# Performance work log

Hardware: AMD Instinct MI355X
Metric: run time of the kernel (lower is better)

The kernel has to match this reference:

```python
import jax, jax.numpy as jnp
import numpy as np

N = 4096          # nodes (= Mamba sequence length)
E_EDGES = 65536   # edges
D = 512           # dim_h (= d_inner, expand=1)
NEXP = 4          # num_experts (cfg.model.num_experts)
DSTATE = 16
DCONV = 4
DTRANK = 32       # ceil(D/16)
EPS = 1e-5


def _silu(x):
    return x * jax.nn.sigmoid(x)


def _bn(h, g, b):
    # BatchNorm1d over node axis (batch statistics)
    mu = h.mean(0)
    var = h.var(0)
    return (h - mu) * jax.lax.rsqrt(var + EPS) * g + b


def _mamba(u, in_w, conv_w, conv_b, x_w, dt_w, dt_b, A_log, Dp, out_w):
    # u: [L, D] single-sequence Mamba(d_model=D, d_state=16, d_conv=4, expand=1)
    L = u.shape[0]
    xz = u @ in_w                      # [L, 2D]
    xc, z = xz[:, :D], xz[:, D:]
    xp = jnp.pad(xc, ((DCONV - 1, 0), (0, 0)))
    xconv = conv_b
    for k in range(DCONV):             # depthwise causal conv, tiny fixed loop
        xconv = xconv + conv_w[:, k] * xp[k:k + L]
    xs = _silu(xconv)                  # [L, D]
    dbc = xs @ x_w                     # [L, DTRANK + 2*DSTATE]
    dt = jax.nn.softplus(dbc[:, :DTRANK] @ dt_w + dt_b)          # [L, D]
    Bm = dbc[:, DTRANK:DTRANK + DSTATE]                          # [L, S]
    Cm = dbc[:, DTRANK + DSTATE:]                                # [L, S]
    A = -jnp.exp(A_log)                                          # [D, S]
    dA = jnp.exp(dt[:, :, None] * A[None])                       # [L, D, S]
    dBu = dt[:, :, None] * Bm[:, None, :] * xs[:, :, None]       # [L, D, S]

    def step(hprev, inp):
        dA_t, dBu_t, C_t = inp
        hn = dA_t * hprev + dBu_t
        return hn, (hn * C_t[None, :]).sum(-1)

    _, ys = jax.lax.scan(step, jnp.zeros((D, DSTATE), u.dtype), (dA, dBu, Cm))
    y = ys + Dp * xs
    return (y * _silu(z)) @ out_w      # [L, D]


def setup_inputs() -> dict:
    key = jax.random.key(0)
    ks = jax.random.split(key, 24)
    s = 1.0 / np.sqrt(D)
    inp = {}
    inp['x'] = jax.random.normal(ks[0], (N, D), jnp.float32)
    inp['edge_index'] = jax.random.randint(ks[1], (2, E_EDGES), 0, N)
    inp['edge_attr'] = jax.random.normal(ks[2], (E_EDGES, D), jnp.float32)
    # GINE nn: Linear(D,D) -> ReLU -> Linear(D,D)
    inp['gin_w1'] = jax.random.normal(ks[3], (D, D)) * s
    inp['gin_b1'] = jnp.zeros((D,))
    inp['gin_w2'] = jax.random.normal(ks[4], (D, D)) * s
    inp['gin_b2'] = jnp.zeros((D,))
    # BatchNorms
    inp['bn1l_g'] = jnp.ones((D,)); inp['bn1l_b'] = jnp.zeros((D,))
    inp['bn1a_g'] = jnp.ones((D,)); inp['bn1a_b'] = jnp.zeros((D,))
    inp['bn2_g'] = jnp.ones((D,)); inp['bn2_b'] = jnp.zeros((D,))
    # gating MLP [D, D//2, NEXP]
    inp['gate_w1'] = jax.random.normal(ks[5], (D, D // 2)) * s
    inp['gate_b1'] = jnp.zeros((D // 2,))
    inp['gate_w2'] = jax.random.normal(ks[6], (D // 2, NEXP)) * (1.0 / np.sqrt(D // 2))
    inp['gate_b2'] = jnp.zeros((NEXP,))
    # stacked per-expert Mamba params
    inp['in_w'] = jax.random.normal(ks[7], (NEXP, D, 2 * D)) * s
    inp['conv_w'] = jax.random.normal(ks[8], (NEXP, D, DCONV)) * 0.5
    inp['conv_b'] = jnp.zeros((NEXP, D))
    inp['x_w'] = jax.random.normal(ks[9], (NEXP, D, DTRANK + 2 * DSTATE)) * s
    inp['dt_w'] = jax.random.normal(ks[10], (NEXP, DTRANK, D)) * (1.0 / np.sqrt(DTRANK))
    inp['dt_b'] = jax.random.normal(ks[11], (NEXP, D)) * 0.1 - 4.0
    A0 = jnp.log(jnp.arange(1, DSTATE + 1, dtype=jnp.float32))
    inp['A_log'] = jnp.broadcast_to(A0, (NEXP, D, DSTATE)).copy()
    inp['Dp'] = jnp.ones((NEXP, D))
    inp['out_w'] = jax.random.normal(ks[12], (NEXP, D, D)) * s
    # FFN
    inp['ff_w1'] = jax.random.normal(ks[13], (D, 2 * D)) * s
    inp['ff_b1'] = jnp.zeros((2 * D,))
    inp['ff_w2'] = jax.random.normal(ks[14], (2 * D, D)) * (1.0 / np.sqrt(2 * D))
    inp['ff_b2'] = jnp.zeros((D,))
    return inp


def reference(x, edge_index, edge_attr,
              gin_w1, gin_b1, gin_w2, gin_b2,
              bn1l_g, bn1l_b, bn1a_g, bn1a_b, bn2_g, bn2_b,
              gate_w1, gate_b1, gate_w2, gate_b2,
              in_w, conv_w, conv_b, x_w, dt_w, dt_b, A_log, Dp, out_w,
              ff_w1, ff_b1, ff_w2, ff_b2):
    h_in = x
    src, dst = edge_index[0], edge_index[1]
    # local GINEConv: nn(x + sum_j relu(x_j + e_ji))
    msg = jax.nn.relu(x[src] + edge_attr)                      # [E, D]
    aggr = jax.ops.segment_sum(msg, dst, num_segments=N)       # [N, D]
    h_local = jax.nn.relu((x + aggr) @ gin_w1 + gin_b1) @ gin_w2 + gin_b2
    h_local = _bn(h_in + h_local, bn1l_g, bn1l_b)
    # gated mixture of Mamba experts
    gate = jax.nn.softmax(jax.nn.relu(x @ gate_w1 + gate_b1) @ gate_w2 + gate_b2, axis=-1)  # [N, NEXP]
    ys = jax.vmap(_mamba, in_axes=(None, 0, 0, 0, 0, 0, 0, 0, 0, 0))(
        x, in_w, conv_w, conv_b, x_w, dt_w, dt_b, A_log, Dp, out_w)  # [NEXP, N, D]
    h_attn = jnp.einsum('ne,end->nd', gate, ys)
    h_attn = _bn(h_in + h_attn, bn1a_g, bn1a_b)
    # fuse + FFN
    h = h_local + h_attn
    ff = jax.nn.relu(h @ ff_w1 + ff_b1) @ ff_w2 + ff_b2
    return _bn(h + ff, bn2_g, bn2_b)
```

## Files before the change

### kernel.cpp

```cpp
#include <hip/hip_runtime.h>
#include <hip/hip_bf16.h>
#include <math.h>

#define N_NODES 4096
#define E_EDGE 65536
#define D 512
#define NEXP 4
#define DSTATE 16
#define DCONV 4
#define DTRANK 32
#define EPS 1e-5f
#define LCHUNK 32
#define NCHUNK (N_NODES / LCHUNK)

typedef __hip_bfloat16 bf16;
typedef short bf16x8 __attribute__((ext_vector_type(8)));
typedef float f32x4 __attribute__((ext_vector_type(4)));
typedef unsigned short u16x4 __attribute__((ext_vector_type(4)));

__device__ __forceinline__ float siluf(float x) { return x / (1.f + __expf(-x)); }
__device__ __forceinline__ float softplusf(float x) {
  return (x > 20.f) ? x : log1pf(__expf(x));
}
__device__ __forceinline__ unsigned short f2bf(float v) {
  bf16 b = __float2bfloat16(v);
  return *reinterpret_cast<unsigned short*>(&b);
}
__device__ __forceinline__ float bfu2f(unsigned short u) {
  bf16 b;
  *reinterpret_cast<unsigned short*>(&b) = u;
  return __bfloat162float(b);
}

__device__ __forceinline__ void gload16(const void* g, void* l) {
  __builtin_amdgcn_global_load_lds(
      (const __attribute__((address_space(1))) void*)g,
      (__attribute__((address_space(3))) void*)l, 16, 0, 0);
}

template <int FN, int EPI, bool STATS>
__global__ __launch_bounds__(256, 2) void mm_k(
    const bf16* __restrict__ A, int lda, long sA,
    const bf16* __restrict__ Bt, int ldb, long sB,
    const float* __restrict__ bias,
    float* __restrict__ Cf, bf16* __restrict__ Cb, int ldc, long sC, int K,
    const float* __restrict__ part, float* __restrict__ sacc) {
  constexpr int BN = FN * 32;
  __shared__ __align__(16) bf16 As[2][128 * 32];
  __shared__ __align__(16) bf16 Bs[2][BN * 32];
  const int z = blockIdx.z;
  A += (size_t)z * sA;
  Bt += (size_t)z * sB;
  const int tid = threadIdx.x;
  const int w = tid >> 6, l = tid & 63;
  const int wr = w >> 1, wc = w & 1;
  const int bm = blockIdx.y * 128, bn = blockIdx.x * BN;

  f32x4 acc[4][FN];
#pragma unroll
  for (int i = 0; i < 4; ++i)
#pragma unroll
    for (int j = 0; j < FN; ++j) acc[i][j] = 0.f;

  const int srow = l >> 2, schunk = l & 3;
  const bf16* gA = A + (size_t)(bm + w * 16 + srow) * lda + schunk * 8;
  const bf16* gB = Bt + (size_t)(bn + w * 16 + srow) * ldb + schunk * 8;

  const int ar = wr * 64 + (l & 15);
  const int br = wc * FN * 16 + (l & 15);
  const int kb = l >> 4;

  auto stage = [&](int b, int k0) {
    gload16(gA + k0, As[b] + w * 512);
    gload16(gA + k0 + (size_t)64 * lda, As[b] + 64 * 32 + w * 512);
    gload16(gB + k0, Bs[b] + w * 512);
    if (FN == 4) gload16(gB + k0 + (size_t)64 * ldb, Bs[b] + 64 * 32 + w * 512);
  };

  stage(0, 0);
  __syncthreads();
  int cur = 0;
  for (int k0 = 0; k0 < K; k0 += 32) {
    if (k0 + 32 < K) stage(cur ^ 1, k0 + 32);
    const bf16x8* Ap = (const bf16x8*)As[cur];
    const bf16x8* Bp = (const bf16x8*)Bs[cur];
    bf16x8 af[4], bfr[FN];
#pragma unroll
    for (int i = 0; i < 4; ++i) af[i] = Ap[(ar + i * 16) * 4 + kb];
#pragma unroll
    for (int j = 0; j < FN; ++j) bfr[j] = Bp[(br + j * 16) * 4 + kb];
#pragma unroll
    for (int i = 0; i < 4; ++i)
#pragma unroll
      for (int j = 0; j < FN; ++j)
        acc[i][j] = __builtin_amdgcn_mfma_f32_16x16x32_bf16(bfr[j], af[i], acc[i][j], 0, 0, 0);
    __syncthreads();
    cur ^= 1;
  }

  if (Cf) Cf += (size_t)z * sC;
  if (Cb) Cb += (size_t)z * sC;
  const int r0 = bm + wr * 64 + (l & 15);
  const int cb0 = bn + wc * FN * 16 + ((l >> 4) << 2);
  f32x4 ssum[FN], ssq[FN];
  if (STATS) {
#pragma unroll
    for (int j = 0; j < FN; ++j) { ssum[j] = 0.f; ssq[j] = 0.f; }
  }
#pragma unroll
  for (int i = 0; i < 4; ++i) {
    const int row = r0 + i * 16;
#pragma unroll
    for (int j = 0; j < FN; ++j) {
      const int col = cb0 + j * 16;
      f32x4 v = acc[i][j];
      if (bias) v += *(const f32x4*)&bias[col];
      if (EPI == 1) {
#pragma unroll
        for (int r = 0; r < 4; ++r) v[r] = fmaxf(v[r], 0.f);
      }
      if (Cf) *(f32x4*)&Cf[(size_t)row * ldc + col] = v;
      if (Cb) {
        u16x4 u;
#pragma unroll
        for (int r = 0; r < 4; ++r) u[r] = f2bf(v[r]);
        *(u16x4*)&Cb[(size_t)row * ldc + col] = u;
      }
      if (STATS) {
        f32x4 p = *(const f32x4*)&part[(size_t)row * ldc + col];
        f32x4 t = v + p;
        ssum[j] += t;
        ssq[j] += t * t;
      }
    }
  }
  if (STATS) {
#pragma unroll
    for (int m = 1; m < 16; m <<= 1) {
#pragma unroll
      for (int j = 0; j < FN; ++j)
#pragma unroll
        for (int r = 0; r < 4; ++r) {
          ssum[j][r] += __shfl_xor(ssum[j][r], m);
          ssq[j][r] += __shfl_xor(ssq[j][r], m);
        }
    }
    if ((l & 15) == 0) {
#pragma unroll
      for (int j = 0; j < FN; ++j)
#pragma unroll
        for (int r = 0; r < 4; ++r) {
          atomicAdd(&sacc[cb0 + j * 16 + r], ssum[j][r]);
          atomicAdd(&sacc[512 + cb0 + j * 16 + r], ssq[j][r]);
        }
    }
  }
}

struct MmArgs {
  const bf16* A[4];
  const bf16* Bt[4];
  const float* bias[4];
  float* Cf[4];
  bf16* Cb[4];
  const float* part[4];
  float* sacc[4];
  long sA[4], sB[4], sC[4];
  int lda[4], ldb[4], ldc[4], K[4], epi[4], stats[4], gx[4], cum[4];
};
__global__ __launch_bounds__(256, 2) void mgemm_k(MmArgs a) {
  __shared__ __align__(16) bf16 As[2][128 * 32];
  __shared__ __align__(16) bf16 Bs[2][64 * 32];
  int b = blockIdx.x;
  int i = 0;
  while (b >= a.cum[i]) ++i;
  int local = b - (i ? a.cum[i - 1] : 0);
  const int perz = a.gx[i] * 32;
  const int z = local / perz;
  const int rem = local - z * perz;
  const int by = rem / a.gx[i];
  const int bx = rem - by * a.gx[i];
  const int lda = a.lda[i], ldb = a.ldb[i], ldc = a.ldc[i], K = a.K[i];
  const bf16* A = a.A[i] + (size_t)z * a.sA[i];
  const bf16* Bt = a.Bt[i] + (size_t)z * a.sB[i];

  const int tid = threadIdx.x;
  const int w = tid >> 6, l = tid & 63;
  const int wr = w >> 1, wc = w & 1;
  const int bm = by * 128, bn = bx * 64;

  f32x4 acc[4][2];
#pragma unroll
  for (int p = 0; p < 4; ++p)
#pragma unroll
    for (int j = 0; j < 2; ++j) acc[p][j] = 0.f;

  const int srow = l >> 2, schunk = l & 3;
  const bf16* gA = A + (size_t)(bm + w * 16 + srow) * lda + schunk * 8;
  const bf16* gB = Bt + (size_t)(bn + w * 16 + srow) * ldb + schunk * 8;

  const int ar = wr * 64 + (l & 15);
  const int br = wc * 32 + (l & 15);
  const int kb = l >> 4;

  auto stage = [&](int bb, int k0) {
    gload16(gA + k0, As[bb] + w * 512);
    gload16(gA + k0 + (size_t)64 * lda, As[bb] + 64 * 32 + w * 512);
    gload16(gB + k0, Bs[bb] + w * 512);
  };

  stage(0, 0);
  __syncthreads();
  int cur = 0;
  for (int k0 = 0; k0 < K; k0 += 32) {
    if (k0 + 32 < K) stage(cur ^ 1, k0 + 32);
    const bf16x8* Ap = (const bf16x8*)As[cur];
    const bf16x8* Bp = (const bf16x8*)Bs[cur];
    bf16x8 af[4], bfr[2];
#pragma unroll
    for (int p = 0; p < 4; ++p) af[p] = Ap[(ar + p * 16) * 4 + kb];
#pragma unroll
    for (int j = 0; j < 2; ++j) bfr[j] = Bp[(br + j * 16) * 4 + kb];
#pragma unroll
    for (int p = 0; p < 4; ++p)
#pragma unroll
      for (int j = 0; j < 2; ++j)
        acc[p][j] = __builtin_amdgcn_mfma_f32_16x16x32_bf16(bfr[j], af[p], acc[p][j], 0, 0, 0);
    __syncthreads();
    cur ^= 1;
  }

  float* Cf = a.Cf[i] ? a.Cf[i] + (size_t)z * a.sC[i] : nullptr;
  bf16* Cb = a.Cb[i] ? a.Cb[i] + (size_t)z * a.sC[i] : nullptr;
  const float* bias = a.bias[i];
  const int epi = a.epi[i], stats = a.stats[i];
  const int r0 = bm + wr * 64 + (l & 15);
  const int cb0 = bn + wc * 32 + ((l >> 4) << 2);
  f32x4 ssum[2], ssq[2];
  ssum[0] = 0.f; ssum[1] = 0.f; ssq[0] = 0.f; ssq[1] = 0.f;
#pragma unroll
  for (int p = 0; p < 4; ++p) {
    const int row = r0 + p * 16;
#pragma unroll
    for (int j = 0; j < 2; ++j) {
      const int col = cb0 + j * 16;
      f32x4 v = acc[p][j];
      if (bias) v += *(const f32x4*)&bias[col];
      if (epi == 1) {
#pragma unroll
        for (int r = 0; r < 4; ++r) v[r] = fmaxf(v[r], 0.f);
      }
      if (Cf) *(f32x4*)&Cf[(size_t)row * ldc + col] = v;
      if (Cb) {
        u16x4 u;
#pragma unroll
        for (int r = 0; r < 4; ++r) u[r] = f2bf(v[r]);
        *(u16x4*)&Cb[(size_t)row * ldc + col] = u;
      }
      if (stats) {
        f32x4 pp = *(const f32x4*)&a.part[i][(size_t)row * ldc + col];
        f32x4 t = v + pp;
        ssum[j] += t;
        ssq[j] += t * t;
      }
    }
  }
  if (stats) {
#pragma unroll
    for (int m = 1; m < 16; m <<= 1) {
#pragma unroll
      for (int j = 0; j < 2; ++j)
#pragma unroll
        for (int r = 0; r < 4; ++r) {
          ssum[j][r] += __shfl_xor(ssum[j][r], m);
          ssq[j][r] += __shfl_xor(ssq[j][r], m);
        }
    }
    if ((l & 15) == 0) {
#pragma unroll
      for (int j = 0; j < 2; ++j)
#pragma unroll
        for (int r = 0; r < 4; ++r) {
          atomicAdd(&a.sacc[i][cb0 + j * 16 + r], ssum[j][r]);
          atomicAdd(&a.sacc[i][512 + cb0 + j * 16 + r], ssq[j][r]);
        }
    }
  }
}

struct WtArgs {
  const float* in[8];
  bf16* out[8];
  int K[8], N[8], ldo[8];
  long sin[8], sout[8];
  int cum[8];
};
__global__ __launch_bounds__(256) void wtrans_all_k(WtArgs a) {
  __shared__ float t[32][33];
  int b = blockIdx.x;
  int i = 0;
  while (b >= a.cum[i]) ++i;
  int local = b - (i ? a.cum[i - 1] : 0);
  const int ntx = a.N[i] / 32;
  const int nty = a.K[i] / 32;
  const int perz = ntx * nty;
  const int z = local / perz;
  const int rem = local - z * perz;
  const int bx = rem % ntx, by = rem / ntx;
  const float* in = a.in[i] + (size_t)z * a.sin[i];
  bf16* out = a.out[i] + (size_t)z * a.sout[i];
  const int N = a.N[i], ldo = a.ldo[i];
  const int n0 = bx * 32, k0 = by * 32;
  const int tx = threadIdx.x & 31, ty = threadIdx.x >> 5;
  for (int r = ty; r < 32; r += 8) t[r][tx] = in[(size_t)(k0 + r) * N + n0 + tx];
  __syncthreads();
  for (int r = ty; r < 32; r += 8)
    out[(size_t)(n0 + r) * ldo + k0 + tx] = __float2bfloat16(t[tx][r]);
}

__global__ void hist_k(const int* __restrict__ ei, int* __restrict__ deg) {
  int e = blockIdx.x * 256 + threadIdx.x;
  if (e < E_EDGE) atomicAdd(&deg[ei[E_EDGE + e]], 1);
}

__global__ __launch_bounds__(1024) void prefix_k(const int* __restrict__ deg,
                                                 int* __restrict__ rowstart) {
  __shared__ int s[1024];
  int t = threadIdx.x;
  int base = t * 4;
  int d0 = deg[base], d1 = deg[base + 1], d2 = deg[base + 2], d3 = deg[base + 3];
  int sum = d0 + d1 + d2 + d3;
  s[t] = sum;
  __syncthreads();
  for (int off = 1; off < 1024; off <<= 1) {
    int v = (t >= off) ? s[t - off] : 0;
    __syncthreads();
    s[t] += v;
    __syncthreads();
  }
  int excl = s[t] - sum;
  rowstart[base] = excl;
  rowstart[base + 1] = excl + d0;
  rowstart[base + 2] = excl + d0 + d1;
  rowstart[base + 3] = excl + d0 + d1 + d2;
}

__global__ void scatter_k(const int* __restrict__ ei, const int* __restrict__ rowstart,
                          int* __restrict__ cnt, int* __restrict__ eid) {
  int e = blockIdx.x * 256 + threadIdx.x;
  if (e < E_EDGE) {
    int dst = ei[E_EDGE + e];
    int slot = rowstart[dst] + atomicAdd(&cnt[dst], 1);
    eid[slot] = e;
  }
}

__global__ __launch_bounds__(256) void aggr_gather_k(
    const float* __restrict__ x, const int* __restrict__ ei, const float* __restrict__ ea,
    const int* __restrict__ rowstart, const int* __restrict__ deg,
    const int* __restrict__ eid, bf16* __restrict__ hpre, bf16* __restrict__ xbf) {
  __shared__ float comb[512];
  const int n = blockIdx.x;
  const int sub = threadIdx.x >> 7;
  const int lane = threadIdx.x & 127;
  const int d4 = lane << 2;
  const int beg = rowstart[n];
  const int end = beg + deg[n];
  f32x4 a = 0.f;
  for (int i = beg + sub; i < end; i += 2) {
    const int e = eid[i];
    const int s = ei[e];
    f32x4 xv = *(const f32x4*)&x[(size_t)s * D + d4];
    f32x4 ev = *(const f32x4*)&ea[(size_t)e * D + d4];
#pragma unroll
    for (int j = 0; j < 4; ++j) a[j] += fmaxf(xv[j] + ev[j], 0.f);
  }
  if (sub == 0) *(f32x4*)&comb[d4] = a;
  __syncthreads();
  if (sub == 1) {
    a += *(const f32x4*)&comb[d4];
    f32x4 xn = *(const f32x4*)&x[(size_t)n * D + d4];
    u16x4 h, xb;
#pragma unroll
    for (int j = 0; j < 4; ++j) {
      h[j] = f2bf(xn[j] + a[j]);
      xb[j] = f2bf(xn[j]);
    }
    *(u16x4*)&hpre[(size_t)n * D + d4] = h;
    *(u16x4*)&xbf[(size_t)n * D + d4] = xb;
  }
}

__device__ __forceinline__ void gate2_body(const float* __restrict__ g1,
                                           const float* __restrict__ w2,
                                           const float* __restrict__ b2,
                                           float* __restrict__ gate, int blk) {
  int row = blk * 4 + (threadIdx.x >> 6);
  int lane = threadIdx.x & 63;
  float a0 = 0.f, a1 = 0.f, a2 = 0.f, a3 = 0.f;
  for (int k = lane; k < 256; k += 64) {
    float v = g1[(size_t)row * 256 + k];
    a0 = fmaf(v, w2[k * 4 + 0], a0);
    a1 = fmaf(v, w2[k * 4 + 1], a1);
    a2 = fmaf(v, w2[k * 4 + 2], a2);
    a3 = fmaf(v, w2[k * 4 + 3], a3);
  }
#pragma unroll
  for (int off = 32; off; off >>= 1) {
    a0 += __shfl_down(a0, off);
    a1 += __shfl_down(a1, off);
    a2 += __shfl_down(a2, off);
    a3 += __shfl_down(a3, off);
  }
  if (lane == 0) {
    float l0 = a0 + b2[0], l1 = a1 + b2[1], l2 = a2 + b2[2], l3 = a3 + b2[3];
    float m = fmaxf(fmaxf(l0, l1), fmaxf(l2, l3));
    float e0 = __expf(l0 - m), e1 = __expf(l1 - m), e2 = __expf(l2 - m), e3 = __expf(l3 - m);
    float s = 1.f / (e0 + e1 + e2 + e3);
    gate[row * 4 + 0] = e0 * s;
    gate[row * 4 + 1] = e1 * s;
    gate[row * 4 + 2] = e2 * s;
    gate[row * 4 + 3] = e3 * s;
  }
}

__global__ __launch_bounds__(256) void gate2_k(const float* __restrict__ g1,
                                               const float* __restrict__ w2,
                                               const float* __restrict__ b2,
                                               float* __restrict__ gate) {
  gate2_body(g1, w2, b2, gate, blockIdx.x);
}

__device__ __forceinline__ void conv_body(const bf16* __restrict__ xz,
                                          const float* __restrict__ cw,
                                          const float* __restrict__ cb,
                                          bf16* __restrict__ xs, int z, int e0, int bx) {
  xz += (size_t)z * N_NODES * 2 * D;
  xs += (size_t)z * N_NODES * D;
  cw += (size_t)(e0 + z) * D * DCONV;
  cb += (size_t)(e0 + z) * D;
  int idx = bx * 256 + threadIdx.x;
  if (idx >= N_NODES * (D / 4)) return;
  int t = idx >> 7;
  int d4 = (idx & 127) << 2;
  float a[4];
#pragma unroll
  for (int j = 0; j < 4; ++j) a[j] = cb[d4 + j];
#pragma unroll
  for (int k = 0; k < DCONV; ++k) {
    int tt = t + k - (DCONV - 1);
    if (tt >= 0) {
      u16x4 v = *(const u16x4*)&xz[(size_t)tt * (2 * D) + d4];
#pragma unroll
      for (int j = 0; j < 4; ++j) a[j] = fmaf(cw[(d4 + j) * DCONV + k], bfu2f(v[j]), a[j]);
    }
  }
  u16x4 o;
#pragma unroll
  for (int j = 0; j < 4; ++j) o[j] = f2bf(siluf(a[j]));
  *(u16x4*)&xs[(size_t)t * D + d4] = o;
}

__global__ void conv_silu_k(const bf16* __restrict__ xz, const float* __restrict__ cw,
                            const float* __restrict__ cb, bf16* __restrict__ xs, int e0) {
  conv_body(xz, cw, cb, xs, blockIdx.y, e0, blockIdx.x);
}

__global__ __launch_bounds__(256) void convgate_k(
    const bf16* __restrict__ xz, const float* __restrict__ cw,
    const float* __restrict__ cb, bf16* __restrict__ xs,
    const float* __restrict__ g1, const float* __restrict__ w2,
    const float* __restrict__ b2, float* __restrict__ gate) {
  if (blockIdx.y == 4) {
    if (blockIdx.x < N_NODES / 4) gate2_body(g1, w2, b2, gate, blockIdx.x);
    return;
  }
  conv_body(xz, cw, cb, xs, blockIdx.y, 0, blockIdx.x);
}

__device__ __forceinline__ void bn_params(const float* acc, int d, float& mu, float& rsig) {
  mu = acc[d] * (1.f / N_NODES);
  float var = acc[512 + d] * (1.f / N_NODES) - mu * mu;
  rsig = rsqrtf(var + EPS);
}

__global__ void norm_k(const float* __restrict__ p, const bf16* __restrict__ q,
                       const float* __restrict__ acc, const float* __restrict__ g,
                       const float* __restrict__ b, float* __restrict__ o) {
  int idx = blockIdx.x * blockDim.x + threadIdx.x;
  if (idx >= N_NODES * (D / 4)) return;
  int d4 = (idx & 127) << 2;
  size_t base = (size_t)idx << 2;
  f32x4 pv = *(const f32x4*)&p[base];
  u16x4 qv = *(const u16x4*)&q[base];
  f32x4 gv = *(const f32x4*)&g[d4];
  f32x4 bv = *(const f32x4*)&b[d4];
  f32x4 ov;
#pragma unroll
  for (int j = 0; j < 4; ++j) {
    float mu, rs;
    bn_params(acc, d4 + j, mu, rs);
    ov[j] = (pv[j] + bfu2f(qv[j]) - mu) * rs * gv[j] + bv[j];
  }
  *(f32x4*)&o[base] = ov;
}

__global__ void bnadd2_k(const float* __restrict__ x, const bf16* __restrict__ hloc,
                         const bf16* __restrict__ hattn, const float* __restrict__ acc1,
                         const float* __restrict__ acc2, const float* __restrict__ g1,
                         const float* __restrict__ b1, const float* __restrict__ g2,
                         const float* __restrict__ b2, float* __restrict__ of,
                         bf16* __restrict__ ob) {
  int idx = blockIdx.x * blockDim.x + threadIdx.x;
  if (idx >= N_NODES * (D / 4)) return;
  int d4 = (idx & 127) << 2;
  size_t base = (size_t)idx << 2;
  f32x4 xv = *(const f32x4*)&x[base];
  u16x4 hl = *(const u16x4*)&hloc[base];
  u16x4 ha = *(const u16x4*)&hattn[base];
  f32x4 g1v = *(const f32x4*)&g1[d4];
  f32x4 b1v = *(const f32x4*)&b1[d4];
  f32x4 g2v = *(const f32x4*)&g2[d4];
  f32x4 b2v = *(const f32x4*)&b2[d4];
  f32x4 ov;
  u16x4 obv;
#pragma unroll
  for (int j = 0; j < 4; ++j) {
    float mu1, rs1, mu2, rs2;
    bn_params(acc1, d4 + j, mu1, rs1);
    bn_params(acc2, d4 + j, mu2, rs2);
    float v = (xv[j] + bfu2f(hl[j]) - mu1) * rs1 * g1v[j] + b1v[j] +
              (xv[j] + bfu2f(ha[j]) - mu2) * rs2 * g2v[j] + b2v[j];
    ov[j] = v;
    obv[j] = f2bf(v);
  }
  *(f32x4*)&of[base] = ov;
  *(u16x4*)&ob[base] = obv;
}

__global__ __launch_bounds__(512) void scanA_k(const bf16* __restrict__ xs,
                                               const float* __restrict__ dbc,
                                               const float* __restrict__ Alog,
                                               const float* __restrict__ dtw,
                                               const float* __restrict__ dtbias,
                                               bf16* __restrict__ dtout,
                                               float* __restrict__ Q,
                                               float* __restrict__ dtsum, int e0) {
  const int z = blockIdx.y;
  xs += (size_t)z * N_NODES * D;
  dbc += (size_t)z * N_NODES * 64;
  Alog += (size_t)(e0 + z) * D * DSTATE;
  dtw += (size_t)(e0 + z) * DTRANK * D;
  dtbias += (size_t)(e0 + z) * D;
  dtout += (size_t)z * N_NODES * D;
  Q += (size_t)z * NCHUNK * D * DSTATE;
  dtsum += (size_t)z * NCHUNK * D;
  int c = blockIdx.x;
  int d = threadIdx.x;
  float wv[DTRANK];
#pragma unroll
  for (int k = 0; k < DTRANK; ++k) wv[k] = dtw[k * D + d];
  const float dtb0 = dtbias[d];
  float As[DSTATE], h[DSTATE];
#pragma unroll
  for (int s = 0; s < DSTATE; ++s) {
    As[s] = -__expf(Alog[d * DSTATE + s]);
    h[s] = 0.f;
  }
  float dts = 0.f;
  int t0 = c * LCHUNK;
  for (int t = t0; t < t0 + LCHUNK; ++t) {
    float acc = dtb0;
#pragma unroll
    for (int k = 0; k < DTRANK; ++k) acc = fmaf(dbc[(size_t)t * 64 + k], wv[k], acc);
    bf16 dtb16 = __float2bfloat16(softplusf(acc));
    dtout[(size_t)t * D + d] = dtb16;
    float dtv = __bfloat162float(dtb16);
    float xv = __bfloat162float(xs[(size_t)t * D + d]);
    float bx = dtv * xv;
    dts += dtv;
#pragma unroll
    for (int s = 0; s < DSTATE; ++s) {
      float Bv = dbc[(size_t)t * 64 + DTRANK + s];
      h[s] = fmaf(__expf(dtv * As[s]), h[s], bx * Bv);
    }
  }
  size_t base = ((size_t)c * D + d) * DSTATE;
#pragma unroll
  for (int s = 0; s < DSTATE; ++s) Q[base + s] = h[s];
  dtsum[c * D + d] = dts;
}

__global__ __launch_bounds__(256) void scanB_k(const float* __restrict__ Q,
                                               const float* __restrict__ dtsum,
                                               const float* __restrict__ Alog,
                                               float* __restrict__ Hin, int e0) {
  const int z = blockIdx.y;
  Q += (size_t)z * NCHUNK * D * DSTATE;
  dtsum += (size_t)z * NCHUNK * D;
  Alog += (size_t)(e0 + z) * D * DSTATE;
  Hin += (size_t)z * NCHUNK * D * DSTATE;
  int idx = blockIdx.x * blockDim.x + threadIdx.x;
  int d = idx >> 4;
  float As = -__expf(Alog[idx]);
  float h = 0.f;
  for (int c = 0; c < NCHUNK; ++c) {
    size_t base = (size_t)c * D * DSTATE + idx;
    Hin[base] = h;
    h = fmaf(__expf(As * dtsum[c * D + d]), h, Q[base]);
  }
}

__global__ __launch_bounds__(512) void scanC_k(const bf16* __restrict__ dt,
                                               const bf16* __restrict__ xs,
                                               const float* __restrict__ dbc,
                                               const float* __restrict__ Alog,
                                               const float* __restrict__ Hin,
                                               const bf16* __restrict__ xz,
                                               const float* __restrict__ Dp,
                                               const float* __restrict__ gate,
                                               bf16* __restrict__ u, int e0) {
  const int z = blockIdx.y;
  dt += (size_t)z * N_NODES * D;
  xs += (size_t)z * N_NODES * D;
  dbc += (size_t)z * N_NODES * 64;
  Alog += (size_t)(e0 + z) * D * DSTATE;
  Hin += (size_t)z * NCHUNK * D * DSTATE;
  xz += (size_t)z * N_NODES * 2 * D;
  Dp += (size_t)(e0 + z) * D;
  u += (size_t)(e0 + z) * 512;
  const int ge = e0 + z;
  int c = blockIdx.x;
  int d = threadIdx.x;
  float As[DSTATE], h[DSTATE];
  size_t base = ((size_t)c * D + d) * DSTATE;
#pragma unroll
  for (int s = 0; s < DSTATE; ++s) {
    As[s] = -__expf(Alog[d * DSTATE + s]);
    h[s] = Hin[base + s];
  }
  float Dv = Dp[d];
  int t0 = c * LCHUNK;
  for (int t = t0; t < t0 + LCHUNK; ++t) {
    float dtv = __bfloat162float(dt[(size_t)t * D + d]);
    float xv = __bfloat162float(xs[(size_t)t * D + d]);
    float bx = dtv * xv;
    float y = 0.f;
#pragma unroll
    for (int s = 0; s < DSTATE; ++s) {
      float Bv = dbc[(size_t)t * 64 + DTRANK + s];
      float Cv = dbc[(size_t)t * 64 + DTRANK + DSTATE + s];
      h[s] = fmaf(__expf(dtv * As[s]), h[s], bx * Bv);
      y = fmaf(h[s], Cv, y);
    }
    float zv = __bfloat162float(xz[(size_t)t * (2 * D) + D + d]);
    float gv = gate[t * NEXP + ge];
    u[(size_t)t * 2048 + d] = __float2bfloat16(gv * (y + Dv * xv) * siluf(zv));
  }
}

extern "C" void kernel_launch(void* const* d_in, const int* in_sizes, int n_in,
                              void* d_out, int out_size, void* d_ws, size_t ws_size,
                              hipStream_t stream) {
  const float* x = (const float*)d_in[0];
  const int* ei = (const int*)d_in[1];
  const float* ea = (const float*)d_in[2];
  const float* gin_w1 = (const float*)d_in[3];
  const float* gin_b1 = (const float*)d_in[4];
  const float* gin_w2 = (const float*)d_in[5];
  const float* gin_b2 = (const float*)d_in[6];
  const float* bn1l_g = (const float*)d_in[7];
  const float* bn1l_b = (const float*)d_in[8];
  const float* bn1a_g = (const float*)d_in[9];
  const float* bn1a_b = (const float*)d_in[10];
  const float* bn2_g = (const float*)d_in[11];
  const float* bn2_b = (const float*)d_in[12];
  const float* gate_w1 = (const float*)d_in[13];
  const float* gate_b1 = (const float*)d_in[14];
  const float* gate_w2 = (const float*)d_in[15];
  const float* gate_b2 = (const float*)d_in[16];
  const float* in_w = (const float*)d_in[17];
  const float* conv_w = (const float*)d_in[18];
  const float* conv_b = (const float*)d_in[19];
  const float* x_w = (const float*)d_in[20];
  const float* dt_w = (const float*)d_in[21];
  const float* dt_b = (const float*)d_in[22];
  const float* A_log = (const float*)d_in[23];
  const float* Dp = (const float*)d_in[24];
  const float* out_w = (const float*)d_in[25];
  const float* ff_w1 = (const float*)d_in[26];
  const float* ff_b1 = (const float*)d_in[27];
  const float* ff_w2 = (const float*)d_in[28];
  const float* ff_b2 = (const float*)d_in[29];
  float* out = (float*)d_out;

  const size_t ND = (size_t)N_NODES * D;
  const size_t NDb = ND / 2;

  const size_t fixed_f = 3 * ND + (size_t)N_NODES * 256 + 16384 + 2490624 + ND + 2048 +
                         81920 + 2 * ND + 4096;
  const size_t per_f = 2 * ND + NDb + (size_t)N_NODES * 64 + NDb +
                       2 * (size_t)NCHUNK * D * DSTATE + (size_t)NCHUNK * D;
  const int EB = (ws_size >= (fixed_f + 4 * per_f + 65536) * sizeof(float)) ? 4 : 1;

  float* ws = (float*)d_ws;
  size_t off = 0;
  auto alloc = [&](size_t n) {
    float* p = ws + off;
    off += (n + 63) & ~(size_t)63;
    return p;
  };
  float* ffo_f = alloc(ND);
  float* pbuf = alloc(ND);
  float* hlocal_f = alloc(ND);
  float* g1 = alloc((size_t)N_NODES * 256);
  float* gate = alloc((size_t)N_NODES * NEXP);
  bf16* gw1t = (bf16*)alloc(131072);
  bf16* gw2t = (bf16*)alloc(131072);
  bf16* gatew1t = (bf16*)alloc(65536);
  bf16* inwt = (bf16*)alloc(1048576);
  bf16* xwt = (bf16*)alloc(65536);
  bf16* outwt_cat = (bf16*)alloc(524288);
  bf16* ffw1t = (bf16*)alloc(262144);
  bf16* ffw2t = (bf16*)alloc(262144);
  int* deg = (int*)alloc(N_NODES);
  int* cnt = (int*)alloc(N_NODES);
  float* accs = alloc(3072);
  int* eid = (int*)alloc(E_EDGE);
  int* rowstart = (int*)alloc(N_NODES);
  float* xbf_f = alloc(NDb);
  float* xz_f = alloc((size_t)EB * ND);
  float* xs_f = alloc((size_t)EB * NDb);
  float* dbc = alloc((size_t)EB * N_NODES * 64);
  float* dtb_f = alloc((size_t)EB * NDb);
  float* Qb = alloc((size_t)EB * NCHUNK * D * DSTATE);
  float* Hin = alloc((size_t)EB * NCHUNK * D * DSTATE);
  float* dtsum = alloc((size_t)EB * NCHUNK * D);
  float* ucat_f = alloc(4 * NDb);
  float* hattn_f = alloc(ND);
  float* acc1 = accs, *acc2 = accs + 1024, *acc3 = accs + 2048;

  bf16* x_bf = (bf16*)xbf_f;
  bf16* hpre_bf = (bf16*)pbuf;
  bf16* t1_bf = (bf16*)(pbuf + NDb);
  bf16* xz_bf = (bf16*)xz_f;
  bf16* xs_bf = (bf16*)xs_f;
  bf16* dt_bf = (bf16*)dtb_f;
  bf16* ucat = (bf16*)ucat_f;
  bf16* hlocal_bf = (bf16*)hlocal_f;
  bf16* hattn_bf = (bf16*)hattn_f;
  bf16* ffo_bf = (bf16*)ffo_f;
  float* hcomb = xz_f;
  bf16* hcomb_bf = (bf16*)(ucat_f);
  bf16* ffh_bf = (bf16*)pbuf;

  const int nelem = N_NODES * D;
  const int ew4 = (nelem / 4 + 255) / 256;

  hipMemsetAsync(deg, 0, (N_NODES + N_NODES + 3072) * sizeof(float), stream);

  WtArgs wa;
  const float* wsrc[8] = {gin_w1, gin_w2, gate_w1, in_w, x_w, out_w, ff_w1, ff_w2};
  bf16* wdst[8] = {gw1t, gw2t, gatew1t, inwt, xwt, outwt_cat, ffw1t, ffw2t};
  int wK[8] = {512, 512, 512, 512, 512, 512, 512, 1024};
  int wN[8] = {512, 512, 256, 1024, 64, 512, 1024, 512};
  int wldo[8] = {512, 512, 512, 512, 512, 2048, 512, 1024};
  long wsin[8] = {0, 0, 0, (long)512 * 1024, (long)512 * 64, (long)512 * 512, 0, 0};
  long wsout[8] = {0, 0, 0, (long)512 * 1024, (long)64 * 512, 512, 0, 0};
  int wz[8] = {1, 1, 1, 4, 4, 4, 1, 1};
  int cum = 0;
  for (int i = 0; i < 8; ++i) {
    wa.in[i] = wsrc[i];
    wa.out[i] = wdst[i];
    wa.K[i] = wK[i];
    wa.N[i] = wN[i];
    wa.ldo[i] = wldo[i];
    wa.sin[i] = wsin[i];
    wa.sout[i] = wsout[i];
    cum += (wN[i] / 32) * (wK[i] / 32) * wz[i];
    wa.cum[i] = cum;
  }
  wtrans_all_k<<<cum, 256, 0, stream>>>(wa);

  hist_k<<<E_EDGE / 256, 256, 0, stream>>>(ei, deg);
  prefix_k<<<1, 1024, 0, stream>>>(deg, rowstart);
  scatter_k<<<E_EDGE / 256, 256, 0, stream>>>(ei, rowstart, cnt, eid);
  aggr_gather_k<<<N_NODES, 256, 0, stream>>>(x, ei, ea, rowstart, deg, eid, hpre_bf, x_bf);

  if (EB == 4) {
    MmArgs m1 = {};
    m1.A[0] = hpre_bf; m1.lda[0] = 512; m1.sA[0] = 0;
    m1.Bt[0] = gw1t; m1.ldb[0] = 512; m1.sB[0] = 0;
    m1.bias[0] = gin_b1; m1.Cb[0] = t1_bf; m1.ldc[0] = 512; m1.sC[0] = 0;
    m1.K[0] = 512; m1.epi[0] = 1; m1.gx[0] = 8;
    m1.A[1] = x_bf; m1.lda[1] = 512; m1.sA[1] = 0;
    m1.Bt[1] = gatew1t; m1.ldb[1] = 512; m1.sB[1] = 0;
    m1.bias[1] = gate_b1; m1.Cf[1] = g1; m1.ldc[1] = 256; m1.sC[1] = 0;
    m1.K[1] = 512; m1.epi[1] = 1; m1.gx[1] = 4;
    m1.A[2] = x_bf; m1.lda[2] = 512; m1.sA[2] = 0;
    m1.Bt[2] = inwt; m1.ldb[2] = 512; m1.sB[2] = (long)512 * 1024;
    m1.Cb[2] = xz_bf; m1.ldc[2] = 1024; m1.sC[2] = (long)N_NODES * 1024;
    m1.K[2] = 512; m1.epi[2] = 0; m1.gx[2] = 16;
    int c1 = 8 * 32;
    m1.cum[0] = c1;
    c1 += 4 * 32;
    m1.cum[1] = c1;
    c1 += 16 * 32 * 4;
    m1.cum[2] = c1;
    m1.cum[3] = c1;
    mgemm_k<<<c1, 256, 0, stream>>>(m1);
    convgate_k<<<dim3(ew4, 5), 256, 0, stream>>>(xz_bf, conv_w, conv_b, xs_bf, g1,
                                                 gate_w2, gate_b2, gate);

    MmArgs m2 = {};
    m2.A[0] = t1_bf; m2.lda[0] = 512; m2.sA[0] = 0;
    m2.Bt[0] = gw2t; m2.ldb[0] = 512; m2.sB[0] = 0;
    m2.bias[0] = gin_b2; m2.Cb[0] = hlocal_bf; m2.ldc[0] = 512; m2.sC[0] = 0;
    m2.K[0] = 512; m2.epi[0] = 0; m2.stats[0] = 1; m2.part[0] = x; m2.sacc[0] = acc1;
    m2.gx[0] = 8;
    m2.A[1] = xs_bf; m2.lda[1] = 512; m2.sA[1] = (long)ND;
    m2.Bt[1] = xwt; m2.ldb[1] = 512; m2.sB[1] = (long)64 * 512;
    m2.Cf[1] = dbc; m2.ldc[1] = 64; m2.sC[1] = (long)N_NODES * 64;
    m2.K[1] = 512; m2.epi[1] = 0; m2.gx[1] = 1;
    int c2 = 8 * 32;
    m2.cum[0] = c2;
    c2 += 1 * 32 * 4;
    m2.cum[1] = c2;
    m2.cum[2] = c2;
    m2.cum[3] = c2;
    mgemm_k<<<c2, 256, 0, stream>>>(m2);

    scanA_k<<<dim3(NCHUNK, 4), 512, 0, stream>>>(xs_bf, dbc, A_log, dt_w, dt_b, dt_bf,
                                                 Qb, dtsum, 0);
    scanB_k<<<dim3((D * DSTATE) / 256, 4), 256, 0, stream>>>(Qb, dtsum, A_log, Hin, 0);
    scanC_k<<<dim3(NCHUNK, 4), 512, 0, stream>>>(dt_bf, xs_bf, dbc, A_log, Hin, xz_bf, Dp,
                                                 gate, ucat, 0);
  } else {
    mm_k<2, 1, false><<<dim3(8, 32, 1), 256, 0, stream>>>(
        hpre_bf, 512, 0, gw1t, 512, 0, gin_b1, nullptr, t1_bf, 512, 0, 512, nullptr,
        nullptr);
    mm_k<2, 0, true><<<dim3(8, 32, 1), 256, 0, stream>>>(
        t1_bf, 512, 0, gw2t, 512, 0, gin_b2, nullptr, hlocal_bf, 512, 0, 512, x, acc1);
    mm_k<2, 1, false><<<dim3(4, 32, 1), 256, 0, stream>>>(
        x_bf, 512, 0, gatew1t, 512, 0, gate_b1, g1, nullptr, 256, 0, 512, nullptr,
        nullptr);
    gate2_k<<<N_NODES / 4, 256, 0, stream>>>(g1, gate_w2, gate_b2, gate);
    for (int e0 = 0; e0 < NEXP; ++e0) {
      mm_k<4, 0, false><<<dim3(8, 32, 1), 256, 0, stream>>>(
          x_bf, 512, 0, inwt + (size_t)e0 * 512 * 1024, 512, 0, nullptr, nullptr, xz_bf,
          1024, 0, 512, nullptr, nullptr);
      conv_silu_k<<<dim3(ew4, 1), 256, 0, stream>>>(xz_bf, conv_w, conv_b, xs_bf, e0);
      mm_k<2, 0, false><<<dim3(1, 32, 1), 256, 0, stream>>>(
          xs_bf, 512, 0, xwt + (size_t)e0 * 64 * 512, 512, 0, nullptr, dbc, nullptr, 64,
          0, 512, nullptr, nullptr);
      scanA_k<<<dim3(NCHUNK, 1), 512, 0, stream>>>(xs_bf, dbc, A_log, dt_w, dt_b, dt_bf,
                                                   Qb, dtsum, e0);
      scanB_k<<<dim3((D * DSTATE) / 256, 1), 256, 0, stream>>>(Qb, dtsum, A_log, Hin, e0);
      scanC_k<<<dim3(NCHUNK, 1), 512, 0, stream>>>(dt_bf, xs_bf, dbc, A_log, Hin, xz_bf,
                                                   Dp, gate, ucat, e0);
    }
  }

  mm_k<2, 0, true><<<dim3(8, 32, 1), 256, 0, stream>>>(
      ucat, 2048, 0, outwt_cat, 2048, 0, nullptr, nullptr, hattn_bf, 512, 0, 2048, x,
      acc2);

  bnadd2_k<<<ew4, 256, 0, stream>>>(x, hlocal_bf, hattn_bf, acc1, acc2, bn1l_g, bn1l_b,
                                    bn1a_g, bn1a_b, hcomb, hcomb_bf);
  mm_k<4, 1, false><<<dim3(8, 32, 1), 256, 0, stream>>>(
      hcomb_bf, 512, 0, ffw1t, 512, 0, ff_b1, nullptr, ffh_bf, 1024, 0, 512, nullptr,
      nullptr);
  mm_k<2, 0, true><<<dim3(8, 32, 1), 256, 0, stream>>>(
      ffh_bf, 1024, 0, ffw2t, 1024, 0, ff_b2, nullptr, ffo_bf, 512, 0, 1024, hcomb, acc3);
  norm_k<<<ew4, 256, 0, stream>>>(hcomb, ffo_bf, acc3, bn2_g, bn2_b, out);
}
```

Before: 429.6 us.

## Replace grouped first-stage GEMM with packed 128x128-tile kernel over concatenated weights

Places the gate and in_proj transposed weights contiguously so x_bf multiplies one concatenated [4352x512] weight matrix. A new dedicated kernel uses 128x128 tiles (1216 blocks), up from 128x64, to do the GIN first linear and this concatenated GEMM, with per-tile epilogue dispatch (relu+bias to bf16, relu+bias to fp32 gate hidden, or raw bf16 xz per expert). The aim is more reuse per A tile, fewer blocks and less per-block argument dispatch. The larger tiles raise register and LDS use, and the hardcoded index maths ties the kernel to these exact shapes.

New measurement: 424.2 us. Within noise of the previous version (-1.3%).

```diff
diff --git a/kernel.cpp b/kernel.cpp
--- a/kernel.cpp
+++ b/kernel.cpp
@@ -153,6 +153,116 @@
           atomicAdd(&sacc[cb0 + j * 16 + r], ssum[j][r]);
           atomicAdd(&sacc[512 + cb0 + j * 16 + r], ssq[j][r]);
         }
+    }
+  }
+}
+
+__global__ __launch_bounds__(256, 2) void g1pack_k(
+    const bf16* __restrict__ hpre, const bf16* __restrict__ xbf,
+    const bf16* __restrict__ gw1t, const bf16* __restrict__ catw,
+    const float* __restrict__ gin_b1, const float* __restrict__ gate_b1,
+    bf16* __restrict__ t1, float* __restrict__ g1, bf16* __restrict__ xz) {
+  __shared__ __align__(16) bf16 As[2][128 * 32];
+  __shared__ __align__(16) bf16 Bs[2][128 * 32];
+  const int b = blockIdx.x;
+  const bool isGin = b < 128;
+  int bm, bnBase;
+  const bf16 *A, *Bt;
+  if (isGin) {
+    bm = (b >> 2) * 128;
+    bnBase = (b & 3) * 128;
+    A = hpre;
+    Bt = gw1t + (size_t)bnBase * 512;
+  } else {
+    const int local = b - 128;
+    bm = (local / 34) * 128;
+    bnBase = (local % 34) * 128;
+    A = xbf;
+    Bt = catw + (size_t)bnBase * 512;
+  }
+  const int tid = threadIdx.x;
+  const int w = tid >> 6, l = tid & 63;
+  const int wr = w >> 1, wc = w & 1;
+
+  f32x4 acc[4][4];
+#pragma unroll
+  for (int i = 0; i < 4; ++i)
+#pragma unroll
+    for (int j = 0; j < 4; ++j) acc[i][j] = 0.f;
+
+  const int srow = l >> 2, schunk = l & 3;
+  const bf16* gA = A + (size_t)(bm + w * 16 + srow) * 512 + schunk * 8;
+  const bf16* gB = Bt + (size_t)(w * 16 + srow) * 512 + schunk * 8;
+
+  const int ar = wr * 64 + (l & 15);
+  const int br = wc * 64 + (l & 15);
+  const int kb = l >> 4;
+
+  auto stage = [&](int bb, int k0) {
+    gload16(gA + k0, As[bb] + w * 512);
+    gload16(gA + k0 + (size_t)64 * 512, As[bb] + 64 * 32 + w * 512);
+    gload16(gB + k0, Bs[bb] + w * 512);
+    gload16(gB + k0 + (size_t)64 * 512, Bs[bb] + 64 * 32 + w * 512);
+  };
+
+  stage(0, 0);
+  __syncthreads();
+  int cur = 0;
+  for (int k0 = 0; k0 < 512; k0 += 32) {
+    if (k0 + 32 < 512) stage(cur ^ 1, k0 + 32);
+    const bf16x8* Ap = (const bf16x8*)As[cur];
+    const bf16x8* Bp = (const bf16x8*)Bs[cur];
+    bf16x8 af[4], bfr[4];
+#pragma unroll
+    for (int i = 0; i < 4; ++i) af[i] = Ap[(ar + i * 16) * 4 + kb];
+#pragma unroll
+    for (int j = 0; j < 4; ++j) bfr[j] = Bp[(br + j * 16) * 4 + kb];
+#pragma unroll
+    for (int i = 0; i < 4; ++i)
+#pragma unroll
+      for (int j = 0; j < 4; ++j)
+        acc[i][j] = __builtin_amdgcn_mfma_f32_16x16x32_bf16(bfr[j], af[i], acc[i][j], 0, 0, 0);
+    __syncthreads();
+    cur ^= 1;
+  }
+
+  const int r0 = bm + wr * 64 + (l & 15);
+  const int c0 = wc * 64 + ((l >> 4) << 2);
+  const bool isGate = (!isGin) && (bnBase < 256);
+  bf16* xz_e = nullptr;
+  int co_base = 0;
+  if (!isGin && !isGate) {
+    const int e = (bnBase - 256) >> 10;
+    xz_e = xz + (size_t)e * N_NODES * 1024;
+    co_base = (bnBase - 256) & 1023;
+  }
+#pragma unroll
+  for (int i = 0; i < 4; ++i) {
+    const int row = r0 + i * 16;
+#pragma unroll
+    for (int j = 0; j < 4; ++j) {
+      const int ct = c0 + j * 16;
+      f32x4 v = acc[i][j];
+      if (isGin) {
+        const int col = bnBase + ct;
+        v += *(const f32x4*)&gin_b1[col];
+        u16x4 u;
+#pragma unroll
+        for (int r = 0; r < 4; ++r) u[r] = f2bf(fmaxf(v[r], 0.f));
+        *(u16x4*)&t1[(size_t)row * 512 + col] = u;
+      } else if (isGate) {
+        const int col = bnBase + ct;
+        v += *(const f32x4*)&gate_b1[col];
+#pragma unroll
+        for (int r = 0; r < 4; ++r) v[r] = fmaxf(v[r], 0.f);
+        *(f32x4*)&g1[(size_t)row * 256 + col] = v;
+      } else {
+        const int co = co_base + ct;
+        u16x4 u;
+#pragma unroll
+        for (int r = 0; r < 4; ++r) u[r] = f2bf(v[r]);
+        *(u16x4*)&xz_e[(size_t)row * 1024 + co] = u;
+      }
     }
   }
 }
@@ -717,8 +827,7 @@
   float* gate = alloc((size_t)N_NODES * NEXP);
   bf16* gw1t = (bf16*)alloc(131072);
   bf16* gw2t = (bf16*)alloc(131072);
-  bf16* gatew1t = (bf16*)alloc(65536);
-  bf16* inwt = (bf16*)alloc(1048576);
+  bf16* catw = (bf16*)alloc(1114112);
   bf16* xwt = (bf16*)alloc(65536);
   bf16* outwt_cat = (bf16*)alloc(524288);
   bf16* ffw1t = (bf16*)alloc(262144);
@@ -750,6 +859,8 @@
   bf16* hlocal_bf = (bf16*)hlocal_f;
   bf16* hattn_bf = (bf16*)hattn_f;
   bf16* ffo_bf = (bf16*)ffo_f;
+  bf16* gatew1t = catw;
+  bf16* inwt = catw + (size_t)256 * 512;
   float* hcomb = xz_f;
   bf16* hcomb_bf = (bf16*)(ucat_f);
   bf16* ffh_bf = (bf16*)pbuf;
@@ -761,12 +872,12 @@
 
   WtArgs wa;
   const float* wsrc[8] = {gin_w1, gin_w2, gate_w1, in_w, x_w, out_w, ff_w1, ff_w2};
-  bf16* wdst[8] = {gw1t, gw2t, gatew1t, inwt, xwt, outwt_cat, ffw1t, ffw2t};
+  bf16* wdst[8] = {gw1t, gw2t, catw, inwt, xwt, outwt_cat, ffw1t, ffw2t};
   int wK[8] = {512, 512, 512, 512, 512, 512, 512, 1024};
   int wN[8] = {512, 512, 256, 1024, 64, 512, 1024, 512};
   int wldo[8] = {512, 512, 512, 512, 512, 2048, 512, 1024};
   long wsin[8] = {0, 0, 0, (long)512 * 1024, (long)512 * 64, (long)512 * 512, 0, 0};
-  long wsout[8] = {0, 0, 0, (long)512 * 1024, (long)64 * 512, 512, 0, 0};
+  long wsout[8] = {0, 0, 0, (long)1024 * 512, (long)64 * 512, 512, 0, 0};
   int wz[8] = {1, 1, 1, 4, 4, 4, 1, 1};
   int cum = 0;
   for (int i = 0; i < 8; ++i) {
@@ -788,27 +899,8 @@
   aggr_gather_k<<<N_NODES, 256, 0, stream>>>(x, ei, ea, rowstart, deg, eid, hpre_bf, x_bf);
 
   if (EB == 4) {
-    MmArgs m1 = {};
-    m1.A[0] = hpre_bf; m1.lda[0] = 512; m1.sA[0] = 0;
-    m1.Bt[0] = gw1t; m1.ldb[0] = 512; m1.sB[0] = 0;
-    m1.bias[0] = gin_b1; m1.Cb[0] = t1_bf; m1.ldc[0] = 512; m1.sC[0] = 0;
-    m1.K[0] = 512; m1.epi[0] = 1; m1.gx[0] = 8;
-    m1.A[1] = x_bf; m1.lda[1] = 512; m1.sA[1] = 0;
-    m1.Bt[1] = gatew1t; m1.ldb[1] = 512; m1.sB[1] = 0;
-    m1.bias[1] = gate_b1; m1.Cf[1] = g1; m1.ldc[1] = 256; m1.sC[1] = 0;
-    m1.K[1] = 512; m1.epi[1] = 1; m1.gx[1] = 4;
-    m1.A[2] = x_bf; m1.lda[2] = 512; m1.sA[2] = 0;
-    m1.Bt[2] = inwt; m1.ldb[2] = 512; m1.sB[2] = (long)512 * 1024;
-    m1.Cb[2] = xz_bf; m1.ldc[2] = 1024; m1.sC[2] = (long)N_NODES * 1024;
-    m1.K[2] = 512; m1.epi[2] = 0; m1.gx[2] = 16;
-    int c1 = 8 * 32;
-    m1.cum[0] = c1;
-    c1 += 4 * 32;
-    m1.cum[1] = c1;
-    c1 += 16 * 32 * 4;
-    m1.cum[2] = c1;
-    m1.cum[3] = c1;
-    mgemm_k<<<c1, 256, 0, stream>>>(m1);
+    g1pack_k<<<1216, 256, 0, stream>>>(hpre_bf, x_bf, gw1t, catw, gin_b1, gate_b1,
+                                       t1_bf, g1, xz_bf);
     convgate_k<<<dim3(ew4, 5), 256, 0, stream>>>(xz_bf, conv_w, conv_b, xs_bf, g1,
                                                  gate_w2, gate_b2, gate);
 
@@ -847,7 +939,7 @@
     gate2_k<<<N_NODES / 4, 256, 0, stream>>>(g1, gate_w2, gate_b2, gate);
     for (int e0 = 0; e0 < NEXP; ++e0) {
       mm_k<4, 0, false><<<dim3(8, 32, 1), 256, 0, stream>>>(
-          x_bf, 512, 0, inwt + (size_t)e0 * 512 * 1024, 512, 0, nullptr, nullptr, xz_bf,
+          x_bf, 512, 0, inwt + (size_t)e0 * 1024 * 512, 512, 0, nullptr, nullptr, xz_bf,
           1024, 0, 512, nullptr, nullptr);
       conv_silu_k<<<dim3(ew4, 1), 256, 0, stream>>>(xz_bf, conv_w, conv_b, xs_bf, e0);
       mm_k<2, 0, false><<<dim3(1, 32, 1), 256, 0, stream>>>(
```
